# Performance work log

Hardware: AMD Instinct MI355X
Metric: run time of the kernel (lower is better)

The kernel has to match this reference:

```python
import jax, jax.numpy as jnp
import numpy as np


def setup_inputs() -> dict:
    key = jax.random.key(0)
    k1, k2, k3, k4 = jax.random.split(key, 4)
    in_features, out_features = 4096, 11008
    n_tokens = 64
    x = jax.random.normal(k1, (n_tokens, in_features), dtype=jnp.float32)
    # int8-valued weights stored as int32 (values in [-128, 127] range subset)
    weight_int = jax.random.randint(k2, (out_features, in_features), 0, 127, dtype=jnp.int32)
    weight_scale = jnp.float32(0.01)
    weight_zero_point = 3  # scalar int zero point
    bias = jax.random.normal(k3, (out_features,), dtype=jnp.float32) * 0.02
    return {
        "x": x,
        "weight_int": weight_int,
        "weight_scale": weight_scale,
        "weight_zero_point": weight_zero_point,
        "bias": bias,
    }


def reference(x, weight_int, weight_scale, weight_zero_point, bias):
    # Dequantize: W = (W_int - zp) * scale, shape [out, in]
    w = (weight_int.astype(jnp.float32) - jnp.float32(weight_zero_point)) * weight_scale
    # F.linear: y = x @ W^T + b
    out = jnp.einsum("ti,oi->to", x, w)
    return out + bias
```

## Files before the change

### kernel.cpp

```cpp
#include <hip/hip_runtime.h>
#include <hip/hip_bf16.h>

typedef __attribute__((ext_vector_type(8))) short short8;
typedef __attribute__((ext_vector_type(4))) float f32x4;
typedef __attribute__((ext_vector_type(4))) int   int4v;

#define IN_F   4096
#define OUT_F  11008
#define COLS   128
#define KSPLIT 8
#define KPART  (IN_F / KSPLIT)
#define BK     64
#define NIT    (KPART / BK)
#define DEPTH  2

__device__ __forceinline__ short bf16_rne(float f) {
    unsigned u = __builtin_bit_cast(unsigned, f);
    u += 0x7FFFu + ((u >> 16) & 1u);
    return (short)(u >> 16);
}

__device__ __forceinline__ void gld16(const void* g, void* l) {
    __builtin_amdgcn_global_load_lds(
        (const __attribute__((address_space(1))) unsigned int*)g,
        (__attribute__((address_space(3))) unsigned int*)l,
        16, 0, 0);
}

__device__ __forceinline__ short8 deq8(int4v q0, int4v q1, int zp) {
    short8 r;
#pragma unroll
    for (int j = 0; j < 4; ++j) {
        r[j]     = (short)(__builtin_bit_cast(unsigned, (float)(q0[j] - zp)) >> 16);
        r[j + 4] = (short)(__builtin_bit_cast(unsigned, (float)(q1[j] - zp)) >> 16);
    }
    return r;
}

__global__ __launch_bounds__(256)
void prep(const float* __restrict__ x, const float* __restrict__ bias,
          unsigned short* __restrict__ xb, float* __restrict__ out) {
    const unsigned cid = blockIdx.x * 256 + threadIdx.x;
    if (blockIdx.x < 128) {
        const int i = cid * 8;
        f32x4 a = *(const f32x4*)(x + i);
        f32x4 b = *(const f32x4*)(x + i + 4);
        short8 o;
#pragma unroll
        for (int j = 0; j < 4; ++j) { o[j] = bf16_rne(a[j]); o[j + 4] = bf16_rne(b[j]); }
        *(short8*)(xb + i) = o;
    }
    const unsigned row = cid / (OUT_F / 8);
    const unsigned o   = (cid - row * (OUT_F / 8)) * 8;
    f32x4 b0 = *(const f32x4*)(bias + o);
    f32x4 b1 = *(const f32x4*)(bias + o + 4);
    float* dst = out + (size_t)row * OUT_F + o;
    *(f32x4*)dst = b0;
    *(f32x4*)(dst + 4) = b1;
}

#define STAGE(IT) do {                                                        \
    const int _s = (IT) & (DEPTH - 1);                                        \
    const int* _wsi = wsrc + (size_t)(IT) * BK;                               \
    gld16(_wsi,             (char*)wt[_s] + tid * 16);                        \
    gld16(_wsi + 32 * IN_F, (char*)wt[_s] + 8192  + tid * 16);                \
    gld16(_wsi + 64 * IN_F, (char*)wt[_s] + 16384 + tid * 16);                \
    gld16(_wsi + 96 * IN_F, (char*)wt[_s] + 24576 + tid * 16);                \
    gld16(xsrc + (size_t)(IT) * BK, (char*)xt[_s] + tid * 16);                \
} while (0)

#define COMPUTE(S) do {                                                       \
    const char* _wb = (const char*)wt[S] + wrow_off;                          \
    int4v _q00 = *(const int4v*)(_wb + cw00);                                 \
    int4v _q01 = *(const int4v*)(_wb + cw01);                                 \
    int4v _q10 = *(const int4v*)(_wb + cw10);                                 \
    int4v _q11 = *(const int4v*)(_wb + cw11);                                 \
    short8 _B0 = deq8(_q00, _q01, zp);                                        \
    short8 _B1 = deq8(_q10, _q11, zp);                                        \
    const char* _xb = (const char*)xt[S] + arow;                              \
    short8 _a;                                                                \
    _a = *(const short8*)(_xb +        ca0);                                  \
    acc0 = __builtin_amdgcn_mfma_f32_16x16x32_bf16(_a, _B0, acc0, 0, 0, 0);   \
    _a = *(const short8*)(_xb +        ca1);                                  \
    acc0 = __builtin_amdgcn_mfma_f32_16x16x32_bf16(_a, _B1, acc0, 0, 0, 0);   \
    _a = *(const short8*)(_xb + 2048 + ca0);                                  \
    acc1 = __builtin_amdgcn_mfma_f32_16x16x32_bf16(_a, _B0, acc1, 0, 0, 0);   \
    _a = *(const short8*)(_xb + 2048 + ca1);                                  \
    acc1 = __builtin_amdgcn_mfma_f32_16x16x32_bf16(_a, _B1, acc1, 0, 0, 0);   \
    _a = *(const short8*)(_xb + 4096 + ca0);                                  \
    acc2 = __builtin_amdgcn_mfma_f32_16x16x32_bf16(_a, _B0, acc2, 0, 0, 0);   \
    _a = *(const short8*)(_xb + 4096 + ca1);                                  \
    acc2 = __builtin_amdgcn_mfma_f32_16x16x32_bf16(_a, _B1, acc2, 0, 0, 0);   \
    _a = *(const short8*)(_xb + 6144 + ca0);                                  \
    acc3 = __builtin_amdgcn_mfma_f32_16x16x32_bf16(_a, _B0, acc3, 0, 0, 0);   \
    _a = *(const short8*)(_xb + 6144 + ca1);                                  \
    acc3 = __builtin_amdgcn_mfma_f32_16x16x32_bf16(_a, _B1, acc3, 0, 0, 0);   \
} while (0)

__global__ __launch_bounds__(512, 4)
void qlin8(const unsigned short* __restrict__ xb, const int* __restrict__ w,
           const float* __restrict__ scale_p, const int* __restrict__ zp_p,
           float* __restrict__ out)
{
    __shared__ __align__(16) int            wt[DEPTH][COLS * BK];
    __shared__ __align__(16) unsigned short xt[DEPTH][64 * BK];

    const int tid  = threadIdx.x;
    const int lane = tid & 63;
    const int wv   = tid >> 6;
    const int l15  = lane & 15;
    const int lg   = lane >> 4;

    const int ob = blockIdx.x >> 3;
    const int kh = blockIdx.x & 7;
    const int o0 = ob * COLS;
    const int kb = kh * KPART;

    const int   zp    = zp_p[0];
    const float scale = scale_p[0];

    const int wr = tid >> 4;
    const int wc = (tid & 15) ^ (wr & 7);
    const int* wsrc = w + (size_t)(o0 + wr) * IN_F + kb + wc * 4;

    const int xr = tid >> 3;
    const int xc = (tid & 7) ^ (xr & 7);
    const unsigned short* xsrc = xb + (size_t)xr * IN_F + kb + xc * 8;

    const int rswz = l15 & 7;
    const int wrow_off = (wv * 16 + l15) * 256;
    const int cw00 = ((lg * 2    ) ^ rswz) * 16;
    const int cw01 = ((lg * 2 + 1) ^ rswz) * 16;
    const int cw10 = ((8 + lg * 2    ) ^ rswz) * 16;
    const int cw11 = ((8 + lg * 2 + 1) ^ rswz) * 16;
    const int arow = l15 * 128;
    const int ca0  = ((lg    ) ^ rswz) * 16;
    const int ca1  = ((4 + lg) ^ rswz) * 16;

    f32x4 acc0 = {0.f, 0.f, 0.f, 0.f};
    f32x4 acc1 = {0.f, 0.f, 0.f, 0.f};
    f32x4 acc2 = {0.f, 0.f, 0.f, 0.f};
    f32x4 acc3 = {0.f, 0.f, 0.f, 0.f};

    STAGE(0);
    STAGE(1);

#pragma unroll
    for (int it = 0; it < NIT; ++it) {
        if (it < NIT - 1) asm volatile("s_waitcnt vmcnt(5)" ::: "memory");
        else              asm volatile("s_waitcnt vmcnt(0)" ::: "memory");
        __builtin_amdgcn_s_barrier();
        COMPUTE(it & 1);
        if (it + 2 < NIT) {
            __builtin_amdgcn_s_barrier();
            STAGE(it + 2);
        }
    }

    {
        const int o = o0 + wv * 16 + l15;
        float* op = out + o;
#pragma unroll
        for (int r = 0; r < 4; ++r) {
            const int tr = lg * 4 + r;
            unsafeAtomicAdd(op + (size_t)(tr     ) * OUT_F, scale * acc0[r]);
            unsafeAtomicAdd(op + (size_t)(tr + 16) * OUT_F, scale * acc1[r]);
            unsafeAtomicAdd(op + (size_t)(tr + 32) * OUT_F, scale * acc2[r]);
            unsafeAtomicAdd(op + (size_t)(tr + 48) * OUT_F, scale * acc3[r]);
        }
    }
}

extern "C" void kernel_launch(void* const* d_in, const int* in_sizes, int n_in,
                              void* d_out, int out_size, void* d_ws, size_t ws_size,
                              hipStream_t stream) {
    const float* x     = (const float*)d_in[0];
    const int*   w     = (const int*)d_in[1];
    const float* scale = (const float*)d_in[2];
    const int*   zp    = (const int*)d_in[3];
    const float* bias  = (const float*)d_in[4];
    float*       out   = (float*)d_out;
    unsigned short* xbf = (unsigned short*)d_ws;

    prep<<<dim3(344), dim3(256), 0, stream>>>(x, bias, xbf, out);
    qlin8<<<dim3((OUT_F / COLS) * KSPLIT), dim3(512), 0, stream>>>(xbf, w, scale, zp, out);
}
```

Before: 48.32 us.

## Load quantized weights straight into registers with triple-buffered rotation instead of LDS

Weight tiles no longer go through shared memory. Each lane now loads its own weight fragments with inline-asm global_load_dwordx4 into one of three register sets, rotating across iterations, and issues the load for iteration it+2 before computing iteration it. Only the activation tile still goes through LDS with global_load_lds. The aim is to cut the LDS write and read traffic and the shared-memory footprint for the dominant weight stream. The cost is 48 extra VGPRs per lane under a 512x4 launch bound, which risks register spills. The inline-asm loads also depend on the hand-written vmcnt accounting to stay correct.

Measured after the change: 49.41 us. 2.3% more time.

```diff
diff --git a/kernel.cpp b/kernel.cpp
--- a/kernel.cpp
+++ b/kernel.cpp
@@ -59,25 +59,30 @@
     *(f32x4*)(dst + 4) = b1;
 }
 
-#define STAGE(IT) do {                                                        \
-    const int _s = (IT) & (DEPTH - 1);                                        \
-    const int* _wsi = wsrc + (size_t)(IT) * BK;                               \
-    gld16(_wsi,             (char*)wt[_s] + tid * 16);                        \
-    gld16(_wsi + 32 * IN_F, (char*)wt[_s] + 8192  + tid * 16);                \
-    gld16(_wsi + 64 * IN_F, (char*)wt[_s] + 16384 + tid * 16);                \
-    gld16(_wsi + 96 * IN_F, (char*)wt[_s] + 24576 + tid * 16);                \
-    gld16(xsrc + (size_t)(IT) * BK, (char*)xt[_s] + tid * 16);                \
+#define WLOAD(IT, S) do {                                                     \
+    const int* _p = wlane + (size_t)(IT) * BK;                                \
+    asm volatile("global_load_dwordx4 %0, %4, off\n\t"                        \
+                 "global_load_dwordx4 %1, %4, off offset:16\n\t"              \
+                 "global_load_dwordx4 %2, %4, off offset:128\n\t"             \
+                 "global_load_dwordx4 %3, %4, off offset:144"                 \
+        : "=&v"(qw##S##0), "=&v"(qw##S##1), "=&v"(qw##S##2), "=&v"(qw##S##3)  \
+        : "v"(_p) : "memory");                                                \
 } while (0)
 
-#define COMPUTE(S) do {                                                       \
-    const char* _wb = (const char*)wt[S] + wrow_off;                          \
-    int4v _q00 = *(const int4v*)(_wb + cw00);                                 \
-    int4v _q01 = *(const int4v*)(_wb + cw01);                                 \
-    int4v _q10 = *(const int4v*)(_wb + cw10);                                 \
-    int4v _q11 = *(const int4v*)(_wb + cw11);                                 \
-    short8 _B0 = deq8(_q00, _q01, zp);                                        \
-    short8 _B1 = deq8(_q10, _q11, zp);                                        \
-    const char* _xb = (const char*)xt[S] + arow;                              \
+#define WLOAD_ROT(IT) do {                                                    \
+    const int _m = (IT) % 3;                                                  \
+    if (_m == 0)      WLOAD(IT, A);                                           \
+    else if (_m == 1) WLOAD(IT, B);                                           \
+    else              WLOAD(IT, C);                                           \
+} while (0)
+
+#define XSTAGE(IT) \
+    gld16(xsrc + (size_t)(IT) * BK, (char*)xt[(IT) & (DEPTH - 1)] + tid * 16)
+
+#define COMPUTE(S, SLOT) do {                                                 \
+    short8 _B0 = deq8(qw##S##0, qw##S##1, zp);                                \
+    short8 _B1 = deq8(qw##S##2, qw##S##3, zp);                                \
+    const char* _xb = (const char*)xt[SLOT] + arow;                           \
     short8 _a;                                                                \
     _a = *(const short8*)(_xb +        ca0);                                  \
     acc0 = __builtin_amdgcn_mfma_f32_16x16x32_bf16(_a, _B0, acc0, 0, 0, 0);   \
@@ -97,12 +102,18 @@
     acc3 = __builtin_amdgcn_mfma_f32_16x16x32_bf16(_a, _B1, acc3, 0, 0, 0);   \
 } while (0)
 
+#define COMPUTE_ROT(IT) do {                                                  \
+    const int _m = (IT) % 3;                                                  \
+    if (_m == 0)      COMPUTE(A, (IT) & 1);                                   \
+    else if (_m == 1) COMPUTE(B, (IT) & 1);                                   \
+    else              COMPUTE(C, (IT) & 1);                                   \
+} while (0)
+
 __global__ __launch_bounds__(512, 4)
-void qlin8(const unsigned short* __restrict__ xb, const int* __restrict__ w,
-           const float* __restrict__ scale_p, const int* __restrict__ zp_p,
-           float* __restrict__ out)
+void qlin11(const unsigned short* __restrict__ xb, const int* __restrict__ w,
+            const float* __restrict__ scale_p, const int* __restrict__ zp_p,
+            float* __restrict__ out)
 {
-    __shared__ __align__(16) int            wt[DEPTH][COLS * BK];
     __shared__ __align__(16) unsigned short xt[DEPTH][64 * BK];
 
     const int tid  = threadIdx.x;
@@ -119,20 +130,13 @@
     const int   zp    = zp_p[0];
     const float scale = scale_p[0];
 
-    const int wr = tid >> 4;
-    const int wc = (tid & 15) ^ (wr & 7);
-    const int* wsrc = w + (size_t)(o0 + wr) * IN_F + kb + wc * 4;
+    const int* wlane = w + (size_t)(o0 + wv * 16 + l15) * IN_F + kb + lg * 8;
 
     const int xr = tid >> 3;
     const int xc = (tid & 7) ^ (xr & 7);
     const unsigned short* xsrc = xb + (size_t)xr * IN_F + kb + xc * 8;
 
     const int rswz = l15 & 7;
-    const int wrow_off = (wv * 16 + l15) * 256;
-    const int cw00 = ((lg * 2    ) ^ rswz) * 16;
-    const int cw01 = ((lg * 2 + 1) ^ rswz) * 16;
-    const int cw10 = ((8 + lg * 2    ) ^ rswz) * 16;
-    const int cw11 = ((8 + lg * 2 + 1) ^ rswz) * 16;
     const int arow = l15 * 128;
     const int ca0  = ((lg    ) ^ rswz) * 16;
     const int ca1  = ((4 + lg) ^ rswz) * 16;
@@ -142,18 +146,26 @@
     f32x4 acc2 = {0.f, 0.f, 0.f, 0.f};
     f32x4 acc3 = {0.f, 0.f, 0.f, 0.f};
 
-    STAGE(0);
-    STAGE(1);
+    int4v qwA0, qwA1, qwA2, qwA3;
+    int4v qwB0, qwB1, qwB2, qwB3;
+    int4v qwC0, qwC1, qwC2, qwC3;
+
+    WLOAD(0, A);
+    XSTAGE(0);
+    WLOAD(1, B);
+    XSTAGE(1);
 
 #pragma unroll
     for (int it = 0; it < NIT; ++it) {
         if (it < NIT - 1) asm volatile("s_waitcnt vmcnt(5)" ::: "memory");
         else              asm volatile("s_waitcnt vmcnt(0)" ::: "memory");
         __builtin_amdgcn_s_barrier();
-        COMPUTE(it & 1);
+        __builtin_amdgcn_sched_barrier(0);
+        if (it + 2 < NIT) WLOAD_ROT(it + 2);
+        COMPUTE_ROT(it);
         if (it + 2 < NIT) {
             __builtin_amdgcn_s_barrier();
-            STAGE(it + 2);
+            XSTAGE(it + 2);
         }
     }
 
@@ -183,5 +195,5 @@
     unsigned short* xbf = (unsigned short*)d_ws;
 
     prep<<<dim3(344), dim3(256), 0, stream>>>(x, bias, xbf, out);
-    qlin8<<<dim3((OUT_F / COLS) * KSPLIT), dim3(512), 0, stream>>>(xbf, w, scale, zp, out);
+    qlin11<<<dim3((OUT_F / COLS) * KSPLIT), dim3(512), 0, stream>>>(xbf, w, scale, zp, out);
 }
```
